# Performance work log

Hardware: AMD Instinct MI355X
Metric: run time of the kernel (lower is better)

The kernel has to match this reference:

```python
import jax, jax.numpy as jnp
import numpy as np
import math

B, S, H, NH, R = 1, 1024, 4096, 32, 16
HD = H // NH
BLOCK = 64
PRUNE_RATIO = 0.5
NF4_TABLE = jnp.array([
    -1.0, -0.6961928009986877, -0.5250730514526367, -0.39491748809814453,
    -0.28444138169288635, -0.18477343022823334, -0.09105003625154495, 0.0,
    0.07958029955625534, 0.16093020141124725, 0.24611230194568634,
    0.33791524171829224, 0.4407098591327667, 0.5626170039176941,
    0.7229568362236023, 1.0], dtype=jnp.float32)


def dequant_nf4(codes, absmax):
    # codes: [out,in] int4 values in [0,16); absmax: per-64-elem block scale
    vals = NF4_TABLE[codes.reshape(-1)]                 # [out*in]
    vals = vals.reshape(-1, BLOCK) * absmax[:, None]    # blockwise rescale
    return vals.reshape(codes.shape)                    # [out,in]


def setup_inputs() -> dict:
    key = jax.random.key(0)
    ks = jax.random.split(key, 32)
    d = {"x": jax.random.normal(ks[0], (B, S, H), dtype=jnp.float32)}
    i = 1
    for n in ("q", "k", "v", "o"):
        d[f"w_{n}_codes"] = jax.random.randint(ks[i], (H, H), 0, 16, dtype=jnp.int32); i += 1
        d[f"w_{n}_absmax"] = jax.random.uniform(ks[i], (H * H // BLOCK,), dtype=jnp.float32) * 0.06; i += 1
        d[f"b_{n}"] = jax.random.normal(ks[i], (H,), dtype=jnp.float32) * 0.01; i += 1
        d[f"w_{n}_lora_a"] = jax.random.normal(ks[i], (H, R), dtype=jnp.float32) * (1.0 / math.sqrt(H)); i += 1
        d[f"w_{n}_lora_b"] = jax.random.normal(ks[i], (R, H), dtype=jnp.float32) * 0.02; i += 1
    causal = jnp.tril(jnp.ones((S, S), dtype=bool))
    d["attention_mask"] = jnp.where(causal, 0.0, -1e9).astype(jnp.float32)[None, None]
    return d


def _proj(x, codes, absmax, b, la, lb):
    w = dequant_nf4(codes, absmax).T          # [in,out]
    main = x @ w + b
    lora_a = x @ la                            # [B,S,R]
    return main + lora_a @ lb, main, lora_a


def _kth_val(t, use_abs=True):
    flat = jnp.abs(t).ravel() if use_abs else t.ravel()
    k = int(t.size * PRUNE_RATIO)
    return jnp.sort(flat)[k - 1]


def reference(x, w_q_codes, w_q_absmax, b_q, w_q_lora_a, w_q_lora_b,
              w_k_codes, w_k_absmax, b_k, w_k_lora_a, w_k_lora_b,
              w_v_codes, w_v_absmax, b_v, w_v_lora_a, w_v_lora_b,
              w_o_codes, w_o_absmax, b_o, w_o_lora_a, w_o_lora_b,
              attention_mask):
    q, _, _ = _proj(x, w_q_codes, w_q_absmax, b_q, w_q_lora_a, w_q_lora_b)
    k, _, _ = _proj(x, w_k_codes, w_k_absmax, b_k, w_k_lora_a, w_k_lora_b)
    v, _, _ = _proj(x, w_v_codes, w_v_absmax, b_v, w_v_lora_a, w_v_lora_b)
    # [B,S,H] -> [B,NH,S,HD]
    qh = q.reshape(B, S, NH, HD).transpose(0, 2, 1, 3)
    kh = k.reshape(B, S, NH, HD).transpose(0, 2, 1, 3)
    vh = v.reshape(B, S, NH, HD).transpose(0, 2, 1, 3)
    s = jnp.einsum("bhqd,bhkd->bhqk", qh, kh) / math.sqrt(HD) + attention_mask
    a = jax.nn.softmax(s, axis=-1)
    o = jnp.einsum("bhqk,bhkd->bhqd", a, vh)
    o = o.transpose(0, 2, 1, 3).reshape(B, S, H)
    o_final, _, _ = _proj(o, w_o_codes, w_o_absmax, b_o, w_o_lora_a, w_o_lora_b)
    # iteration < 10 branch: magnitude-pruning thresholds via kth smallest value
    kth_vals = jnp.stack([
        _kth_val(x), _kth_val(qh), _kth_val(kh), _kth_val(vh),
        _kth_val(a, use_abs=False), _kth_val(o)])
    return o_final, kth_vals
```

## Files before the change

### kernel.cpp

```cpp
#include <hip/hip_runtime.h>

#define S_LEN  1024
#define H_DIM  4096
#define NHEAD  32
#define HEAD_D 128
#define RANK   16
#define KE3    4160
#define KEO    4128
#define TOTP   ((long)NHEAD * S_LEN * S_LEN)

typedef __bf16 bf16x8 __attribute__((ext_vector_type(8)));
typedef float  f32x4  __attribute__((ext_vector_type(4)));
typedef unsigned short ushort8v __attribute__((ext_vector_type(8)));

#define GLOAD_LDS16(g, l) __builtin_amdgcn_global_load_lds( \
    (const __attribute__((address_space(1))) unsigned int*)(g), \
    (__attribute__((address_space(3))) unsigned int*)(l), 16, 0, 0)

__device__ const float NF4_TAB[16] = {
    -1.0f, -0.6961928009986877f, -0.5250730514526367f, -0.39491748809814453f,
    -0.28444138169288635f, -0.18477343022823334f, -0.09105003625154495f, 0.0f,
    0.07958029955625534f, 0.16093020141124725f, 0.24611230194568634f,
    0.33791524171829224f, 0.4407098591327667f, 0.5626170039176941f,
    0.7229568362236023f, 1.0f};

__device__ __forceinline__ unsigned short f2bf(float f) {
    unsigned int u = __builtin_bit_cast(unsigned int, f);
    u = (u + 0x7FFFu + ((u >> 16) & 1u)) >> 16;
    return (unsigned short)u;
}

__device__ __forceinline__ float bf2f(unsigned short s) {
    return __builtin_bit_cast(float, (unsigned int)s << 16);
}

__device__ __forceinline__ void dequant_body(
    const int* __restrict__ codes, const float* __restrict__ absmax,
    unsigned short* __restrict__ out, long i, int ostride) {
    int4 c0 = *(const int4*)(codes + i);
    int4 c1 = *(const int4*)(codes + i + 4);
    float am = absmax[i >> 6];
    long orow = i >> 12;
    int  col  = (int)(i & 4095);
    ushort8v r;
    r[0] = f2bf(NF4_TAB[c0.x] * am);
    r[1] = f2bf(NF4_TAB[c0.y] * am);
    r[2] = f2bf(NF4_TAB[c0.z] * am);
    r[3] = f2bf(NF4_TAB[c0.w] * am);
    r[4] = f2bf(NF4_TAB[c1.x] * am);
    r[5] = f2bf(NF4_TAB[c1.y] * am);
    r[6] = f2bf(NF4_TAB[c1.z] * am);
    r[7] = f2bf(NF4_TAB[c1.w] * am);
    *(ushort8v*)(out + orow * ostride + col) = r;
}

__global__ __launch_bounds__(256) void prep_weights(
    const int* __restrict__ c0, const int* __restrict__ c1,
    const int* __restrict__ c2, const int* __restrict__ c3,
    const float* __restrict__ a0, const float* __restrict__ a1,
    const float* __restrict__ a2, const float* __restrict__ a3,
    const float* __restrict__ lb0, const float* __restrict__ lb1,
    const float* __restrict__ lb2, const float* __restrict__ lb3,
    const float* __restrict__ b0, const float* __restrict__ b1,
    const float* __restrict__ b2,
    unsigned short* __restrict__ wqkv, unsigned short* __restrict__ wo,
    float* __restrict__ bias3, long n) {
    int p = blockIdx.y;
    long bx = blockIdx.x;
    if (bx < 8192) {
        const int* codes = (p == 0) ? c0 : (p == 1) ? c1 : (p == 2) ? c2 : c3;
        const float* am  = (p == 0) ? a0 : (p == 1) ? a1 : (p == 2) ? a2 : a3;
        long i = (bx * 256 + threadIdx.x) * 8;
        if (i >= n) return;
        if (p < 3) dequant_body(codes, am, wqkv + (size_t)p * H_DIM * KE3, i, KE3);
        else       dequant_body(codes, am, wo, i, KEO);
    } else {
        long g = (bx - 8192) * 256 + threadIdx.x;
        if (p < 3) {
            int row = (int)(g >> 6), c = (int)(g & 63);
            const float* lb = (p == 0) ? lb0 : (p == 1) ? lb1 : lb2;
            unsigned int r = (unsigned int)(c - 16 * p);
            float v = (r < 16u) ? lb[r * H_DIM + row] : 0.f;
            wqkv[(size_t)p * H_DIM * KE3 + (long)row * KE3 + 4096 + c] = f2bf(v);
            if (g < H_DIM) {
                const float* bp = (p == 0) ? b0 : (p == 1) ? b1 : b2;
                bias3[(size_t)p * H_DIM + g] = bp[g];
            }
        } else {
            if (g >= (long)H_DIM * 32) return;
            int row = (int)(g >> 5), c = (int)(g & 31);
            float v = (c < 16) ? lb3[c * H_DIM + row] : 0.f;
            wo[(long)row * KEO + 4096 + c] = f2bf(v);
        }
    }
}

__global__ __launch_bounds__(256) void cast_lora(
    const float* __restrict__ x, const float* __restrict__ la0,
    const float* __restrict__ la1, const float* __restrict__ la2,
    unsigned short* __restrict__ xb_ext) {
    __shared__ float xs[4096];
    int m = blockIdx.x, tid = threadIdx.x;
    const float* xr = x + (long)m * H_DIM;
    int c = tid * 16;
    float4 f0 = *(const float4*)(xr + c);
    float4 f1 = *(const float4*)(xr + c + 4);
    float4 f2 = *(const float4*)(xr + c + 8);
    float4 f3 = *(const float4*)(xr + c + 12);
    *(float4*)(xs + c)      = f0;
    *(float4*)(xs + c + 4)  = f1;
    *(float4*)(xs + c + 8)  = f2;
    *(float4*)(xs + c + 12) = f3;
    ushort8v r0, r1;
    r0[0] = f2bf(f0.x); r0[1] = f2bf(f0.y); r0[2] = f2bf(f0.z); r0[3] = f2bf(f0.w);
    r0[4] = f2bf(f1.x); r0[5] = f2bf(f1.y); r0[6] = f2bf(f1.z); r0[7] = f2bf(f1.w);
    r1[0] = f2bf(f2.x); r1[1] = f2bf(f2.y); r1[2] = f2bf(f2.z); r1[3] = f2bf(f2.w);
    r1[4] = f2bf(f3.x); r1[5] = f2bf(f3.y); r1[6] = f2bf(f3.z); r1[7] = f2bf(f3.w);
    unsigned short* orow = xb_ext + (long)m * KE3 + c;
    *(ushort8v*)orow = r0;
    *(ushort8v*)(orow + 8) = r1;
    __syncthreads();
    int w = tid >> 6, lane = tid & 63;
    if (w < 3) {
        const float* la = (w == 0) ? la0 : (w == 1) ? la1 : la2;
        float s[16];
#pragma unroll
        for (int r = 0; r < 16; ++r) s[r] = 0.f;
        for (int k = lane; k < H_DIM; k += 64) {
            float xv = xs[k];
            const float4* lr = (const float4*)(la + (long)k * RANK);
            float4 q0 = lr[0], q1 = lr[1], q2 = lr[2], q3 = lr[3];
            s[0] += xv * q0.x;  s[1] += xv * q0.y;  s[2] += xv * q0.z;  s[3] += xv * q0.w;
            s[4] += xv * q1.x;  s[5] += xv * q1.y;  s[6] += xv * q1.z;  s[7] += xv * q1.w;
            s[8] += xv * q2.x;  s[9] += xv * q2.y;  s[10] += xv * q2.z; s[11] += xv * q2.w;
            s[12] += xv * q3.x; s[13] += xv * q3.y; s[14] += xv * q3.z; s[15] += xv * q3.w;
        }
        for (int off = 32; off; off >>= 1)
#pragma unroll
            for (int r = 0; r < 16; ++r) s[r] += __shfl_xor(s[r], off);
        if (lane == 0)
#pragma unroll
            for (int r = 0; r < 16; ++r)
                xb_ext[(long)m * KE3 + 4096 + 16 * w + r] = f2bf(s[r]);
    }
}

__global__ void transpose_bf16_kernel(const unsigned short* __restrict__ v,
                                      unsigned short* __restrict__ vt) {
    __shared__ unsigned short tile[32][33];
    int c0 = blockIdx.x * 32, s0 = blockIdx.y * 32;
    int tx = threadIdx.x, ty = threadIdx.y;
    tile[ty][tx] = v[(long)(s0 + ty) * H_DIM + c0 + tx];
    __syncthreads();
    vt[(long)(c0 + ty) * S_LEN + s0 + tx] = tile[tx][ty];
}

__global__ __launch_bounds__(256) void lora_ao_kernel(
    unsigned short* __restrict__ ob_ext, const float* __restrict__ la) {
    int m = blockIdx.x;
    const unsigned short* xr = ob_ext + (long)m * KEO;
    int tid = threadIdx.x, lane = tid & 63, wid = tid >> 6;
    float s[4] = {0.f, 0.f, 0.f, 0.f};
    for (int k = lane; k < H_DIM; k += 64) {
        float xv = bf2f(xr[k]);
        const float* lr = la + (long)k * RANK + wid * 4;
        s[0] += xv * lr[0]; s[1] += xv * lr[1];
        s[2] += xv * lr[2]; s[3] += xv * lr[3];
    }
    for (int off = 32; off; off >>= 1)
        for (int r = 0; r < 4; ++r) s[r] += __shfl_down(s[r], off);
    if (lane == 0)
        for (int r = 0; r < 4; ++r)
            ob_ext[(long)m * KEO + 4096 + wid * 4 + r] = f2bf(s[r]);
}

__global__ __launch_bounds__(256) void gemm_nt(
    const unsigned short* __restrict__ A, const unsigned short* __restrict__ B,
    void* __restrict__ Cv, void* __restrict__ Cv2, const float* __restrict__ bias,
    int K, int lda, int ldb, int ldc,
    long strideA, long strideB, long strideC, float alpha, int mode, int obf) {
    int bm, bn;
    int k0s = 0, k0e = K;
    if (mode == 1) {
        int i = blockIdx.x;
        int tm = (int)((sqrtf(8.f * i + 1.f) - 1.f) * 0.5f);
        if ((tm + 1) * (tm + 2) / 2 <= i) tm++;
        if (tm * (tm + 1) / 2 > i) tm--;
        int tn = i - tm * (tm + 1) / 2;
        bm = tm * 128; bn = tn * 128;
    } else {
        bm = blockIdx.y * 128; bn = blockIdx.x * 128;
        if (mode == 2) { int kl = bm + 128; if (kl < k0e) k0e = kl; }
    }
    const unsigned short* Ab = A;
    const unsigned short* Bb = B;
    long coff = 0;
    void* Cuse = Cv;
    if (mode == 3) {
        int Kh = (K / 2) & ~31;
        k0s = blockIdx.z ? Kh : 0;
        k0e = blockIdx.z ? K : Kh;
        Cuse = blockIdx.z ? Cv2 : Cv;
    } else {
        Ab += (long)blockIdx.z * strideA;
        Bb += (long)blockIdx.z * strideB;
        coff = (long)blockIdx.z * strideC;
    }
    __shared__ unsigned short As[128][32];
    __shared__ unsigned short Bs[128][32];
    const int tid = threadIdx.x;
    const int lane = tid & 63, wid = tid >> 6;
    const int wm = (wid >> 1) * 64, wn = (wid & 1) * 64;
    const int sr = wid * 16 + (lane >> 2);
    const int sc = (lane & 3) * 8;
    const unsigned short* gA0 = Ab + (long)(bm + sr) * lda + sc;
    const unsigned short* gA1 = gA0 + (long)64 * lda;
    const unsigned short* gB0 = Bb + (long)(bn + sr) * ldb + sc;
    const unsigned short* gB1 = gB0 + (long)64 * ldb;
    unsigned short* lA0 = &As[wid * 16][0];
    unsigned short* lA1 = &As[64 + wid * 16][0];
    unsigned short* lB0 = &Bs[wid * 16][0];
    unsigned short* lB1 = &Bs[64 + wid * 16][0];
    f32x4 acc[4][4] = {};
    const int kq = (lane >> 4) * 8;
    const int rr = lane & 15;
    for (int k0 = k0s; k0 < k0e; k0 += 32) {
        GLOAD_LDS16(gA0 + k0, lA0);
        GLOAD_LDS16(gA1 + k0, lA1);
        GLOAD_LDS16(gB0 + k0, lB0);
        GLOAD_LDS16(gB1 + k0, lB1);
        __syncthreads();
        bf16x8 af[4], bfr[4];
        for (int i = 0; i < 4; ++i) {
            uint4 ta = *(const uint4*)&As[wm + i * 16 + rr][kq];
            uint4 tb = *(const uint4*)&Bs[wn + i * 16 + rr][kq];
            af[i]  = __builtin_bit_cast(bf16x8, ta);
            bfr[i] = __builtin_bit_cast(bf16x8, tb);
        }
        for (int i = 0; i < 4; ++i)
            for (int j = 0; j < 4; ++j)
                acc[i][j] = __builtin_amdgcn_mfma_f32_16x16x32_bf16(
                    af[i], bfr[j], acc[i][j], 0, 0, 0);
        __syncthreads();
    }
    const int cr = (lane >> 4) * 4;
    const int cc = lane & 15;
    float bv[4];
#pragma unroll
    for (int j = 0; j < 4; ++j)
        bv[j] = bias ? bias[(long)blockIdx.z * H_DIM + bn + wn + j * 16 + cc] : 0.f;
    if (obf) {
        unsigned short* Cb = (unsigned short*)Cuse + coff;
        for (int i = 0; i < 4; ++i)
            for (int j = 0; j < 4; ++j) {
                unsigned short* cp = Cb + (long)(bm + wm + i * 16 + cr) * ldc
                                        + (bn + wn + j * 16 + cc);
                for (int r = 0; r < 4; ++r)
                    cp[(long)r * ldc] = f2bf(acc[i][j][r] * alpha + bv[j]);
            }
    } else {
        float* Cb = (float*)Cuse + coff;
        for (int i = 0; i < 4; ++i)
            for (int j = 0; j < 4; ++j) {
                float* cp = Cb + (long)(bm + wm + i * 16 + cr) * ldc
                               + (bn + wn + j * 16 + cc);
                for (int r = 0; r < 4; ++r)
                    cp[(long)r * ldc] = acc[i][j][r] * alpha + bv[j];
            }
    }
}

__global__ __launch_bounds__(256) void combine_kernel(
    float* __restrict__ out, const float* __restrict__ part,
    const float* __restrict__ bias) {
    long idx = ((long)blockIdx.x * 256 + threadIdx.x) * 4;
    int n = (int)(idx & 4095);
    float4 o = *(float4*)(out + idx);
    float4 p = *(const float4*)(part + idx);
    float4 b = *(const float4*)(bias + n);
    o.x += p.x + b.x; o.y += p.y + b.y; o.z += p.z + b.z; o.w += p.w + b.w;
    *(float4*)(out + idx) = o;
}

__global__ __launch_bounds__(256) void softmax_causal(float* __restrict__ scores) {
    long rowbase = (long)blockIdx.x * S_LEN;
    int i = blockIdx.x & (S_LEN - 1);
    int tid = threadIdx.x, lane = tid & 63, wid = tid >> 6;
    float* row = scores + rowbase;
    int L = i + 1;
    float v[4];
    float mx = -1e30f;
    for (int t = 0; t < 4; ++t) {
        int j = tid + (t << 8);
        v[t] = (j < L) ? row[j] : -1e30f;
        mx = fmaxf(mx, v[t]);
    }
    for (int off = 32; off; off >>= 1) mx = fmaxf(mx, __shfl_xor(mx, off));
    __shared__ float red[4], red2[4];
    if (lane == 0) red[wid] = mx;
    __syncthreads();
    mx = fmaxf(fmaxf(red[0], red[1]), fmaxf(red[2], red[3]));
    float e[4], sum = 0.f;
    for (int t = 0; t < 4; ++t) {
        int j = tid + (t << 8);
        e[t] = (j < L) ? __expf(v[t] - mx) : 0.f;
        sum += e[t];
    }
    for (int off = 32; off; off >>= 1) sum += __shfl_xor(sum, off);
    if (lane == 0) red2[wid] = sum;
    __syncthreads();
    sum = red2[0] + red2[1] + red2[2] + red2[3];
    float inv = 1.f / sum;
    unsigned short* prow = (unsigned short*)scores + rowbase * 2;
    for (int t = 0; t < 4; ++t) {
        int j = tid + (t << 8);
        prow[j] = f2bf(e[t] * inv);
    }
}

__global__ __launch_bounds__(256, 2) void hist6(
    const float* __restrict__ x, const unsigned short* __restrict__ qkv,
    const unsigned short* __restrict__ ob, const unsigned short* __restrict__ P,
    unsigned int* __restrict__ hist) {
    __shared__ unsigned int lh[16384];
    const long SH = (long)S_LEN * H_DIM;
    int t = threadIdx.x, ten = blockIdx.y;
    unsigned int* gh = hist + (long)ten * 16384;
    for (int b = t; b < 16384; b += 256) lh[b] = 0u;
    __syncthreads();
    long i = (long)blockIdx.x * 256 + t;
    long stride = (long)gridDim.x * 256;
    if (ten == 0) {
        for (; i < SH / 4; i += stride) {
            float4 v = *(const float4*)(x + i * 4);
            unsigned int u0 = (__builtin_bit_cast(unsigned int, v.x) & 0x7FFFFFFFu) >> 16;
            unsigned int u1 = (__builtin_bit_cast(unsigned int, v.y) & 0x7FFFFFFFu) >> 16;
            unsigned int u2 = (__builtin_bit_cast(unsigned int, v.z) & 0x7FFFFFFFu) >> 16;
            unsigned int u3 = (__builtin_bit_cast(unsigned int, v.w) & 0x7FFFFFFFu) >> 16;
            atomicAdd(&lh[u0 < 16384u ? u0 : 16383u], 1u);
            atomicAdd(&lh[u1 < 16384u ? u1 : 16383u], 1u);
            atomicAdd(&lh[u2 < 16384u ? u2 : 16383u], 1u);
            atomicAdd(&lh[u3 < 16384u ? u3 : 16383u], 1u);
        }
    } else if (ten <= 3) {
        const unsigned short* src = qkv + (size_t)(ten - 1) * SH;
        for (; i < SH / 8; i += stride) {
            ushort8v v = ((const ushort8v*)src)[i];
#pragma unroll
            for (int j = 0; j < 8; ++j) {
                unsigned int u = v[j] & 0x7FFFu;
                atomicAdd(&lh[u < 16384u ? u : 16383u], 1u);
            }
        }
    } else if (ten == 4) {
        for (; i < SH / 8; i += stride) {
            long off = (i >> 9) * KEO + ((i & 511) << 3);
            ushort8v v = *(const ushort8v*)(ob + off);
#pragma unroll
            for (int j = 0; j < 8; ++j) {
                unsigned int u = v[j] & 0x7FFFu;
                atomicAdd(&lh[u < 16384u ? u : 16383u], 1u);
            }
        }
    } else {
        unsigned int zc = 0;
        for (; i < TOTP / 8; i += stride) {
            long r = i >> 7;
            int c = (int)(i & 127) * 8;
            ushort8v v = *(const ushort8v*)(P + (r << 11) + c);
#pragma unroll
            for (int j = 0; j < 8; ++j) {
                unsigned int b = v[j];
                if (b == 0) zc++;
                else atomicAdd(&lh[b < 16384u ? b : 16383u], 1u);
            }
        }
        if (zc) atomicAdd(&lh[0], zc);
    }
    __syncthreads();
    for (int b = t; b < 16384; b += 256) {
        unsigned int c = lh[b];
        if (c) atomicAdd(&gh[b], c);
    }
}

__global__ __launch_bounds__(256) void scan6(
    const unsigned int* __restrict__ hist, float* __restrict__ out_kth) {
    int ten = blockIdx.x;
    const unsigned int* h = hist + (long)ten * 16384;
    __shared__ unsigned int part[256];
    int t = threadIdx.x;
    unsigned int s = 0;
    for (int b = 0; b < 64; ++b) s += h[t * 64 + b];
    part[t] = s;
    __syncthreads();
    if (t == 0) {
        long k = (ten == 5) ? TOTP / 2 : (long)S_LEN * H_DIM / 2;
        long c = 0;
        int ch = 0;
        for (; ch < 256; ++ch) {
            if (c + (long)part[ch] >= k) break;
            c += part[ch];
        }
        int bin = ch * 64;
        for (;; ++bin) {
            unsigned int hv = h[bin];
            if (c + (long)hv >= k) break;
            c += hv;
        }
        int slot = (ten == 4) ? 5 : (ten == 5) ? 4 : ten;
        out_kth[slot] = __builtin_bit_cast(float, (unsigned int)bin << 16);
    }
}

extern "C" void kernel_launch(void* const* d_in, const int* in_sizes, int n_in,
                              void* d_out, int out_size, void* d_ws, size_t ws_size,
                              hipStream_t stream) {
    (void)in_sizes; (void)n_in; (void)out_size; (void)ws_size;
    const float* x = (const float*)d_in[0];
    const int*   wcodes[4] = {(const int*)d_in[1], (const int*)d_in[6],
                              (const int*)d_in[11], (const int*)d_in[16]};
    const float* wabs[4]   = {(const float*)d_in[2], (const float*)d_in[7],
                              (const float*)d_in[12], (const float*)d_in[17]};
    const float* bias[4]   = {(const float*)d_in[3], (const float*)d_in[8],
                              (const float*)d_in[13], (const float*)d_in[18]};
    const float* lA[4]     = {(const float*)d_in[4], (const float*)d_in[9],
                              (const float*)d_in[14], (const float*)d_in[19]};
    const float* lB[4]     = {(const float*)d_in[5], (const float*)d_in[10],
                              (const float*)d_in[15], (const float*)d_in[20]};

    char* wp = (char*)d_ws;
    auto alloc = [&](size_t bytes) {
        char* p = wp; wp += (bytes + 255) & ~(size_t)255; return p;
    };
    const size_t SH  = (size_t)S_LEN * H_DIM;
    const long   nW  = (long)H_DIM * H_DIM;
    unsigned short* xb_ext = (unsigned short*)alloc((size_t)S_LEN * KE3 * 2);
    unsigned short* qkvb   = (unsigned short*)alloc(3 * SH * 2);
    unsigned short* vT     = (unsigned short*)alloc(SH * 2);
    unsigned short* ob_ext = (unsigned short*)alloc((size_t)S_LEN * KEO * 2);
    unsigned short* Wd_ext = (unsigned short*)alloc((size_t)H_DIM * KEO * 2);
    float*        opart  = (float*)alloc(SH * 4);
    float*        bias3  = (float*)alloc(3 * H_DIM * 4);
    unsigned int* hist   = (unsigned int*)alloc(6 * 16384 * 4);
    float* scores = (float*)alloc((size_t)NHEAD * S_LEN * S_LEN * 4);
    unsigned short* Wqkv_ext = (unsigned short*)scores;

    float* out_final = (float*)d_out;
    float* out_kth   = out_final + SH;

    unsigned short* qb = qkvb;
    unsigned short* kb = qkvb + SH;
    unsigned short* vb = qkvb + 2 * SH;

    prep_weights<<<dim3(9216, 4), 256, 0, stream>>>(
        wcodes[0], wcodes[1], wcodes[2], wcodes[3],
        wabs[0], wabs[1], wabs[2], wabs[3],
        lB[0], lB[1], lB[2], lB[3],
        bias[0], bias[1], bias[2],
        Wqkv_ext, Wd_ext, bias3, nW);

    cast_lora<<<S_LEN, 256, 0, stream>>>(x, lA[0], lA[1], lA[2], xb_ext);

    gemm_nt<<<dim3(32, 8, 3), 256, 0, stream>>>(
        xb_ext, Wqkv_ext, qkvb, nullptr, bias3, KE3, KE3, KE3, H_DIM,
        0, (long)H_DIM * KE3, (long)SH, 1.0f, 0, 1);

    transpose_bf16_kernel<<<dim3(H_DIM / 32, S_LEN / 32), dim3(32, 32), 0, stream>>>(vb, vT);

    gemm_nt<<<dim3(36, 1, NHEAD), 256, 0, stream>>>(
        qb, kb, scores, nullptr, nullptr, HEAD_D, H_DIM, H_DIM, S_LEN,
        128, 128, (long)S_LEN * S_LEN, 0.08838834764831845f, 1, 0);

    softmax_causal<<<NHEAD * S_LEN, 256, 0, stream>>>(scores);

    gemm_nt<<<dim3(1, 8, NHEAD), 256, 0, stream>>>(
        (const unsigned short*)scores, vT, ob_ext, nullptr, nullptr, S_LEN,
        2 * S_LEN, S_LEN, KEO,
        (long)S_LEN * 2 * S_LEN, (long)HEAD_D * S_LEN, 128, 1.0f, 2, 1);

    lora_ao_kernel<<<S_LEN, 256, 0, stream>>>(ob_ext, lA[3]);

    gemm_nt<<<dim3(32, 8, 2), 256, 0, stream>>>(
        ob_ext, Wd_ext, out_final, opart, nullptr, KEO, KEO, KEO, H_DIM,
        0, 0, 0, 1.0f, 3, 0);

    combine_kernel<<<4096, 256, 0, stream>>>(out_final, opart, bias[3]);

    hipMemsetAsync(hist, 0, 6 * 16384 * 4, stream);
    hist6<<<dim3(256, 6), 256, 0, stream>>>(
        x, qkvb, ob_ext, (const unsigned short*)scores, hist);
    scan6<<<6, 256, 0, stream>>>(hist, out_kth);
}
```

Baseline: 805.1 us.

## Store attention scores as bf16, fuse cast/memset into prep, rebalance histogram blocks

```diff
diff --git a/kernel.cpp b/kernel.cpp
--- a/kernel.cpp
+++ b/kernel.cpp
@@ -63,85 +63,98 @@
     const float* __restrict__ lb2, const float* __restrict__ lb3,
     const float* __restrict__ b0, const float* __restrict__ b1,
     const float* __restrict__ b2,
+    const float* __restrict__ x, const float* __restrict__ la0,
+    const float* __restrict__ la1, const float* __restrict__ la2,
     unsigned short* __restrict__ wqkv, unsigned short* __restrict__ wo,
-    float* __restrict__ bias3, long n) {
+    float* __restrict__ bias3, unsigned short* __restrict__ xb_ext,
+    unsigned int* __restrict__ hist, long n) {
+    __shared__ float xs[4096];
     int p = blockIdx.y;
     long bx = blockIdx.x;
+    int tid = threadIdx.x;
     if (bx < 8192) {
         const int* codes = (p == 0) ? c0 : (p == 1) ? c1 : (p == 2) ? c2 : c3;
         const float* am  = (p == 0) ? a0 : (p == 1) ? a1 : (p == 2) ? a2 : a3;
-        long i = (bx * 256 + threadIdx.x) * 8;
+        long i = (bx * 256 + tid) * 8;
         if (i >= n) return;
         if (p < 3) dequant_body(codes, am, wqkv + (size_t)p * H_DIM * KE3, i, KE3);
         else       dequant_body(codes, am, wo, i, KEO);
-    } else {
-        long g = (bx - 8192) * 256 + threadIdx.x;
-        if (p < 3) {
-            int row = (int)(g >> 6), c = (int)(g & 63);
-            const float* lb = (p == 0) ? lb0 : (p == 1) ? lb1 : lb2;
-            unsigned int r = (unsigned int)(c - 16 * p);
-            float v = (r < 16u) ? lb[r * H_DIM + row] : 0.f;
-            wqkv[(size_t)p * H_DIM * KE3 + (long)row * KE3 + 4096 + c] = f2bf(v);
-            if (g < H_DIM) {
-                const float* bp = (p == 0) ? b0 : (p == 1) ? b1 : b2;
-                bias3[(size_t)p * H_DIM + g] = bp[g];
+        return;
+    }
+    if (p < 3) {
+        if (bx >= 9216) return;
+        long g = (bx - 8192) * 256 + tid;
+        int row = (int)(g >> 6), c = (int)(g & 63);
+        const float* lb = (p == 0) ? lb0 : (p == 1) ? lb1 : lb2;
+        unsigned int r = (unsigned int)(c - 16 * p);
+        float v = (r < 16u) ? lb[r * H_DIM + row] : 0.f;
+        wqkv[(size_t)p * H_DIM * KE3 + (long)row * KE3 + 4096 + c] = f2bf(v);
+        if (g < H_DIM) {
+            const float* bp = (p == 0) ? b0 : (p == 1) ? b1 : b2;
+            bias3[(size_t)p * H_DIM + g] = bp[g];
+        }
+        return;
+    }
+    if (bx < 8704) {
+        long g = (bx - 8192) * 256 + tid;
+        if (g >= (long)H_DIM * 32) return;
+        int row = (int)(g >> 5), c = (int)(g & 31);
+        float v = (c < 16) ? lb3[c * H_DIM + row] : 0.f;
+        wo[(long)row * KEO + 4096 + c] = f2bf(v);
+        return;
+    }
+    if (bx < 9088) {
+        long g = (bx - 8704) * 256 + tid;
+        if (g < 6 * 16384) hist[g] = 0u;
+        return;
+    }
+    if (bx < 9216) return;
+    int mbase = 2 * (int)(bx - 9216);
+    for (int rr = 0; rr < 2; ++rr) {
+        int m = mbase + rr;
+        const float* xr = x + (long)m * H_DIM;
+        int c = tid * 16;
+        float4 f0 = *(const float4*)(xr + c);
+        float4 f1 = *(const float4*)(xr + c + 4);
+        float4 f2 = *(const float4*)(xr + c + 8);
+        float4 f3 = *(const float4*)(xr + c + 12);
+        *(float4*)(xs + c)      = f0;
+        *(float4*)(xs + c + 4)  = f1;
+        *(float4*)(xs + c + 8)  = f2;
+        *(float4*)(xs + c + 12) = f3;
+        ushort8v r0, r1;
+        r0[0] = f2bf(f0.x); r0[1] = f2bf(f0.y); r0[2] = f2bf(f0.z); r0[3] = f2bf(f0.w);
+        r0[4] = f2bf(f1.x); r0[5] = f2bf(f1.y); r0[6] = f2bf(f1.z); r0[7] = f2bf(f1.w);
+        r1[0] = f2bf(f2.x); r1[1] = f2bf(f2.y); r1[2] = f2bf(f2.z); r1[3] = f2bf(f2.w);
+        r1[4] = f2bf(f3.x); r1[5] = f2bf(f3.y); r1[6] = f2bf(f3.z); r1[7] = f2bf(f3.w);
+        unsigned short* orow = xb_ext + (long)m * KE3 + c;
+        *(ushort8v*)orow = r0;
+        *(ushort8v*)(orow + 8) = r1;
+        __syncthreads();
+        int w = tid >> 6, lane = tid & 63;
+        if (w < 3) {
+            const float* la = (w == 0) ? la0 : (w == 1) ? la1 : la2;
+            float s[16];
+#pragma unroll
+            for (int r = 0; r < 16; ++r) s[r] = 0.f;
+            for (int k = lane; k < H_DIM; k += 64) {
+                float xv = xs[k];
+                const float4* lr = (const float4*)(la + (long)k * RANK);
+                float4 q0 = lr[0], q1 = lr[1], q2 = lr[2], q3 = lr[3];
+                s[0] += xv * q0.x;  s[1] += xv * q0.y;  s[2] += xv * q0.z;  s[3] += xv * q0.w;
+                s[4] += xv * q1.x;  s[5] += xv * q1.y;  s[6] += xv * q1.z;  s[7] += xv * q1.w;
+                s[8] += xv * q2.x;  s[9] += xv * q2.y;  s[10] += xv * q2.z; s[11] += xv * q2.w;
+                s[12] += xv * q3.x; s[13] += xv * q3.y; s[14] += xv * q3.z; s[15] += xv * q3.w;
             }
-        } else {
-            if (g >= (long)H_DIM * 32) return;
-            int row = (int)(g >> 5), c = (int)(g & 31);
-            float v = (c < 16) ? lb3[c * H_DIM + row] : 0.f;
-            wo[(long)row * KEO + 4096 + c] = f2bf(v);
-        }
-    }
-}
-
-__global__ __launch_bounds__(256) void cast_lora(
-    const float* __restrict__ x, const float* __restrict__ la0,
-    const float* __restrict__ la1, const float* __restrict__ la2,
-    unsigned short* __restrict__ xb_ext) {
-    __shared__ float xs[4096];
-    int m = blockIdx.x, tid = threadIdx.x;
-    const float* xr = x + (long)m * H_DIM;
-    int c = tid * 16;
-    float4 f0 = *(const float4*)(xr + c);
-    float4 f1 = *(const float4*)(xr + c + 4);
-    float4 f2 = *(const float4*)(xr + c + 8);
-    float4 f3 = *(const float4*)(xr + c + 12);
-    *(float4*)(xs + c)      = f0;
-    *(float4*)(xs + c + 4)  = f1;
-    *(float4*)(xs + c + 8)  = f2;
-    *(float4*)(xs + c + 12) = f3;
-    ushort8v r0, r1;
-    r0[0] = f2bf(f0.x); r0[1] = f2bf(f0.y); r0[2] = f2bf(f0.z); r0[3] = f2bf(f0.w);
-    r0[4] = f2bf(f1.x); r0[5] = f2bf(f1.y); r0[6] = f2bf(f1.z); r0[7] = f2bf(f1.w);
-    r1[0] = f2bf(f2.x); r1[1] = f2bf(f2.y); r1[2] = f2bf(f2.z); r1[3] = f2bf(f2.w);
-    r1[4] = f2bf(f3.x); r1[5] = f2bf(f3.y); r1[6] = f2bf(f3.z); r1[7] = f2bf(f3.w);
-    unsigned short* orow = xb_ext + (long)m * KE3 + c;
-    *(ushort8v*)orow = r0;
-    *(ushort8v*)(orow + 8) = r1;
-    __syncthreads();
-    int w = tid >> 6, lane = tid & 63;
-    if (w < 3) {
-        const float* la = (w == 0) ? la0 : (w == 1) ? la1 : la2;
-        float s[16];
-#pragma unroll
-        for (int r = 0; r < 16; ++r) s[r] = 0.f;
-        for (int k = lane; k < H_DIM; k += 64) {
-            float xv = xs[k];
-            const float4* lr = (const float4*)(la + (long)k * RANK);
-            float4 q0 = lr[0], q1 = lr[1], q2 = lr[2], q3 = lr[3];
-            s[0] += xv * q0.x;  s[1] += xv * q0.y;  s[2] += xv * q0.z;  s[3] += xv * q0.w;
-            s[4] += xv * q1.x;  s[5] += xv * q1.y;  s[6] += xv * q1.z;  s[7] += xv * q1.w;
-            s[8] += xv * q2.x;  s[9] += xv * q2.y;  s[10] += xv * q2.z; s[11] += xv * q2.w;
-            s[12] += xv * q3.x; s[13] += xv * q3.y; s[14] += xv * q3.z; s[15] += xv * q3.w;
-        }
-        for (int off = 32; off; off >>= 1)
-#pragma unroll
-            for (int r = 0; r < 16; ++r) s[r] += __shfl_xor(s[r], off);
-        if (lane == 0)
-#pragma unroll
-            for (int r = 0; r < 16; ++r)
-                xb_ext[(long)m * KE3 + 4096 + 16 * w + r] = f2bf(s[r]);
+            for (int off = 32; off; off >>= 1)
+#pragma unroll
+                for (int r = 0; r < 16; ++r) s[r] += __shfl_xor(s[r], off);
+            if (lane == 0)
+#pragma unroll
+                for (int r = 0; r < 16; ++r)
+                    xb_ext[(long)m * KE3 + 4096 + 16 * w + r] = f2bf(s[r]);
+        }
+        __syncthreads();
     }
 }
 
@@ -282,39 +295,42 @@
     *(float4*)(out + idx) = o;
 }
 
-__global__ __launch_bounds__(256) void softmax_causal(float* __restrict__ scores) {
-    long rowbase = (long)blockIdx.x * S_LEN;
-    int i = blockIdx.x & (S_LEN - 1);
+__global__ __launch_bounds__(256) void softmax_causal(unsigned short* __restrict__ scores16) {
+    int b = blockIdx.x;
+    int h = b >> 9, pr = b & 511;
     int tid = threadIdx.x, lane = tid & 63, wid = tid >> 6;
-    float* row = scores + rowbase;
-    int L = i + 1;
-    float v[4];
-    float mx = -1e30f;
-    for (int t = 0; t < 4; ++t) {
-        int j = tid + (t << 8);
-        v[t] = (j < L) ? row[j] : -1e30f;
-        mx = fmaxf(mx, v[t]);
-    }
-    for (int off = 32; off; off >>= 1) mx = fmaxf(mx, __shfl_xor(mx, off));
     __shared__ float red[4], red2[4];
-    if (lane == 0) red[wid] = mx;
-    __syncthreads();
-    mx = fmaxf(fmaxf(red[0], red[1]), fmaxf(red[2], red[3]));
-    float e[4], sum = 0.f;
-    for (int t = 0; t < 4; ++t) {
-        int j = tid + (t << 8);
-        e[t] = (j < L) ? __expf(v[t] - mx) : 0.f;
-        sum += e[t];
-    }
-    for (int off = 32; off; off >>= 1) sum += __shfl_xor(sum, off);
-    if (lane == 0) red2[wid] = sum;
-    __syncthreads();
-    sum = red2[0] + red2[1] + red2[2] + red2[3];
-    float inv = 1.f / sum;
-    unsigned short* prow = (unsigned short*)scores + rowbase * 2;
-    for (int t = 0; t < 4; ++t) {
-        int j = tid + (t << 8);
-        prow[j] = f2bf(e[t] * inv);
+    for (int half = 0; half < 2; ++half) {
+        int i = half ? (S_LEN - 1 - pr) : pr;
+        unsigned short* row = scores16 + ((long)h * S_LEN + i) * S_LEN;
+        int L = i + 1;
+        float v[4];
+        float mx = -1e30f;
+        for (int t = 0; t < 4; ++t) {
+            int j = tid + (t << 8);
+            v[t] = (j < L) ? bf2f(row[j]) : -1e30f;
+            mx = fmaxf(mx, v[t]);
+        }
+        for (int off = 32; off; off >>= 1) mx = fmaxf(mx, __shfl_xor(mx, off));
+        if (lane == 0) red[wid] = mx;
+        __syncthreads();
+        mx = fmaxf(fmaxf(red[0], red[1]), fmaxf(red[2], red[3]));
+        float e[4], sum = 0.f;
+        for (int t = 0; t < 4; ++t) {
+            int j = tid + (t << 8);
+            e[t] = (j < L) ? __expf(v[t] - mx) : 0.f;
+            sum += e[t];
+        }
+        for (int off = 32; off; off >>= 1) sum += __shfl_xor(sum, off);
+        if (lane == 0) red2[wid] = sum;
+        __syncthreads();
+        sum = red2[0] + red2[1] + red2[2] + red2[3];
+        float inv = 1.f / sum;
+        for (int t = 0; t < 4; ++t) {
+            int j = tid + (t << 8);
+            row[j] = f2bf(e[t] * inv);
+        }
+        __syncthreads();
     }
 }
 
@@ -324,12 +340,20 @@
     unsigned int* __restrict__ hist) {
     __shared__ unsigned int lh[16384];
     const long SH = (long)S_LEN * H_DIM;
-    int t = threadIdx.x, ten = blockIdx.y;
+    int t = threadIdx.x;
+    int b = blockIdx.x;
+    int ten, b0, nblk;
+    if (b < 256)      { ten = 0; b0 = 0;   nblk = 256; }
+    else if (b < 384) { ten = 1; b0 = 256; nblk = 128; }
+    else if (b < 512) { ten = 2; b0 = 384; nblk = 128; }
+    else if (b < 640) { ten = 3; b0 = 512; nblk = 128; }
+    else if (b < 768) { ten = 4; b0 = 640; nblk = 128; }
+    else              { ten = 5; b0 = 768; nblk = 768; }
     unsigned int* gh = hist + (long)ten * 16384;
-    for (int b = t; b < 16384; b += 256) lh[b] = 0u;
+    for (int k = t; k < 16384; k += 256) lh[k] = 0u;
     __syncthreads();
-    long i = (long)blockIdx.x * 256 + t;
-    long stride = (long)gridDim.x * 256;
+    long i = (long)(b - b0) * 256 + t;
+    long stride = (long)nblk * 256;
     if (ten == 0) {
         for (; i < SH / 4; i += stride) {
             float4 v = *(const float4*)(x + i * 4);
@@ -365,22 +389,20 @@
     } else {
         unsigned int zc = 0;
         for (; i < TOTP / 8; i += stride) {
-            long r = i >> 7;
-            int c = (int)(i & 127) * 8;
-            ushort8v v = *(const ushort8v*)(P + (r << 11) + c);
+            ushort8v v = ((const ushort8v*)P)[i];
 #pragma unroll
             for (int j = 0; j < 8; ++j) {
-                unsigned int b = v[j];
-                if (b == 0) zc++;
-                else atomicAdd(&lh[b < 16384u ? b : 16383u], 1u);
+                unsigned int bb = v[j];
+                if (bb == 0) zc++;
+                else atomicAdd(&lh[bb < 16384u ? bb : 16383u], 1u);
             }
         }
         if (zc) atomicAdd(&lh[0], zc);
     }
     __syncthreads();
-    for (int b = t; b < 16384; b += 256) {
-        unsigned int c = lh[b];
-        if (c) atomicAdd(&gh[b], c);
+    for (int k = t; k < 16384; k += 256) {
+        unsigned int c = lh[k];
+        if (c) atomicAdd(&gh[k], c);
     }
 }
 
@@ -443,8 +465,10 @@
     float*        opart  = (float*)alloc(SH * 4);
     float*        bias3  = (float*)alloc(3 * H_DIM * 4);
     unsigned int* hist   = (unsigned int*)alloc(6 * 16384 * 4);
-    float* scores = (float*)alloc((size_t)NHEAD * S_LEN * S_LEN * 4);
-    unsigned short* Wqkv_ext = (unsigned short*)scores;
+    char* bigbuf = alloc((size_t)NHEAD * S_LEN * S_LEN * 2 > (size_t)3 * H_DIM * KE3 * 2
+                         ? (size_t)NHEAD * S_LEN * S_LEN * 2 : (size_t)3 * H_DIM * KE3 * 2);
+    unsigned short* Wqkv_ext = (unsigned short*)bigbuf;
+    unsigned short* scores16 = (unsigned short*)bigbuf;
 
     float* out_final = (float*)d_out;
     float* out_kth   = out_final + SH;
@@ -453,14 +477,13 @@
     unsigned short* kb = qkvb + SH;
     unsigned short* vb = qkvb + 2 * SH;
 
-    prep_weights<<<dim3(9216, 4), 256, 0, stream>>>(
+    prep_weights<<<dim3(9728, 4), 256, 0, stream>>>(
         wcodes[0], wcodes[1], wcodes[2], wcodes[3],
         wabs[0], wabs[1], wabs[2], wabs[3],
         lB[0], lB[1], lB[2], lB[3],
         bias[0], bias[1], bias[2],
-        Wqkv_ext, Wd_ext, bias3, nW);
-
-    cast_lora<<<S_LEN, 256, 0, stream>>>(x, lA[0], lA[1], lA[2], xb_ext);
+        x, lA[0], lA[1], lA[2],
+        Wqkv_ext, Wd_ext, bias3, xb_ext, hist, nW);
 
     gemm_nt<<<dim3(32, 8, 3), 256, 0, stream>>>(
         xb_ext, Wqkv_ext, qkvb, nullptr, bias3, KE3, KE3, KE3, H_DIM,
@@ -469,15 +492,15 @@
     transpose_bf16_kernel<<<dim3(H_DIM / 32, S_LEN / 32), dim3(32, 32), 0, stream>>>(vb, vT);
 
     gemm_nt<<<dim3(36, 1, NHEAD), 256, 0, stream>>>(
-        qb, kb, scores, nullptr, nullptr, HEAD_D, H_DIM, H_DIM, S_LEN,
-        128, 128, (long)S_LEN * S_LEN, 0.08838834764831845f, 1, 0);
-
-    softmax_causal<<<NHEAD * S_LEN, 256, 0, stream>>>(scores);
+        qb, kb, scores16, nullptr, nullptr, HEAD_D, H_DIM, H_DIM, S_LEN,
+        128, 128, (long)S_LEN * S_LEN, 0.08838834764831845f, 1, 1);
+
+    softmax_causal<<<NHEAD * S_LEN / 2, 256, 0, stream>>>(scores16);
 
     gemm_nt<<<dim3(1, 8, NHEAD), 256, 0, stream>>>(
-        (const unsigned short*)scores, vT, ob_ext, nullptr, nullptr, S_LEN,
-        2 * S_LEN, S_LEN, KEO,
-        (long)S_LEN * 2 * S_LEN, (long)HEAD_D * S_LEN, 128, 1.0f, 2, 1);
+        scores16, vT, ob_ext, nullptr, nullptr, S_LEN,
+        S_LEN, S_LEN, KEO,
+        (long)S_LEN * S_LEN, (long)HEAD_D * S_LEN, 128, 1.0f, 2, 1);
 
     lora_ao_kernel<<<S_LEN, 256, 0, stream>>>(ob_ext, lA[3]);
 
@@ -487,8 +510,6 @@
 
     combine_kernel<<<4096, 256, 0, stream>>>(out_final, opart, bias[3]);
 
-    hipMemsetAsync(hist, 0, 6 * 16384 * 4, stream);
-    hist6<<<dim3(256, 6), 256, 0, stream>>>(
-        x, qkvb, ob_ext, (const unsigned short*)scores, hist);
+    hist6<<<1536, 256, 0, stream>>>(x, qkvb, ob_ext, scores16, hist);
     scan6<<<6, 256, 0, stream>>>(hist, out_kth);
 }
```

Measured after the change: 890.6 us. 1.11x slower.
